# Optimization experiments

Hardware: AMD Instinct MI355X
Metric: run time of the kernel (lower is better)

The kernel has to match this reference:

```python
import jax, jax.numpy as jnp
import numpy as np

D = 1024
HID = D // 2          # 512
HLEN = 15
IN_DIM = 4
B, N = 32, 512
EPS = 1e-5


def setup_inputs() -> dict:
    key = jax.random.key(0)
    ks = jax.random.split(key, 16)
    inp = {
        "tokens": jax.random.normal(ks[0], (B, N, D), dtype=jnp.float32),
        "history_traj": jax.random.normal(ks[1], (B, N, HLEN, IN_DIM), dtype=jnp.float32),
        "history_abs": jax.random.normal(ks[2], (B, N, 2), dtype=jnp.float32),
        "ego_speed": jax.random.uniform(ks[3], (B,), dtype=jnp.float32),
        "gps_confidence": jax.random.uniform(ks[4], (B,), dtype=jnp.float32),
        # LSTM params (PyTorch layout: gates stacked i,f,g,o along dim 0)
        "W_ih": jax.random.normal(ks[5], (4 * HID, IN_DIM), dtype=jnp.float32) * (1.0 / np.sqrt(IN_DIM)),
        "W_hh": jax.random.normal(ks[6], (4 * HID, HID), dtype=jnp.float32) * (1.0 / np.sqrt(HID)),
        "b_ih": jnp.zeros((4 * HID,), dtype=jnp.float32),
        "b_hh": jnp.zeros((4 * HID,), dtype=jnp.float32),
        "W_rel": jax.random.normal(ks[7], (D, HID), dtype=jnp.float32) * (0.1 / np.sqrt(HID)),
        "W_abs": jax.random.normal(ks[8], (D, 2), dtype=jnp.float32) * 0.1,
        "W_g1": jax.random.normal(ks[9], (16, 2), dtype=jnp.float32) * 0.5,
        "b_g1": jnp.zeros((16,), dtype=jnp.float32),
        "W_g2": jax.random.normal(ks[10], (1, 16), dtype=jnp.float32) * 0.25,
        "b_g2": jnp.zeros((1,), dtype=jnp.float32),
        "gamma": jnp.ones((D,), dtype=jnp.float32),
        "beta": jnp.zeros((D,), dtype=jnp.float32),
    }
    return inp


def _lstm_final_hidden(x, W_ih, W_hh, b_ih, b_hh):
    """x: (BN, H, in) -> final hidden state (BN, HID). PyTorch gate order i,f,g,o."""
    BN = x.shape[0]
    # precompute input contribution for all steps: (H, BN, 4*HID)
    xg = jnp.einsum('bhi,gi->hbg', x, W_ih) + (b_ih + b_hh)

    def step(carry, xg_t):
        h, c = carry
        gates = xg_t + h @ W_hh.T  # (BN, 4*HID)
        i, f, g, o = jnp.split(gates, 4, axis=-1)
        i = jax.nn.sigmoid(i)
        f = jax.nn.sigmoid(f)
        g = jnp.tanh(g)
        o = jax.nn.sigmoid(o)
        c = f * c + i * g
        h = o * jnp.tanh(c)
        return (h, c), None

    h0 = jnp.zeros((BN, HID), dtype=x.dtype)
    c0 = jnp.zeros((BN, HID), dtype=x.dtype)
    (h, _), _ = jax.lax.scan(step, (h0, c0), xg)
    return h


def reference(tokens, history_traj, history_abs, ego_speed, gps_confidence,
              W_ih, W_hh, b_ih, b_hh, W_rel, W_abs, W_g1, b_g1, W_g2, b_g2,
              gamma, beta):
    Bv, Nv, Dv = tokens.shape
    Hv = history_traj.shape[2]
    traj_flat = history_traj.reshape(Bv * Nv, Hv, -1)
    h_n = _lstm_final_hidden(traj_flat, W_ih, W_hh, b_ih, b_hh)  # (B*N, HID)
    h_rel = (h_n @ W_rel.T).reshape(Bv, Nv, Dv)                  # (B, N, D)
    h_abs = history_abs @ W_abs.T                                # (B, N, D)
    conf = jnp.stack([ego_speed, gps_confidence], axis=-1)       # (B, 2)
    gate = jax.nn.relu(conf @ W_g1.T + b_g1) @ W_g2.T + b_g2     # (B, 1)
    alpha = jax.nn.sigmoid(gate)[:, None, :]                     # (B, 1, 1)
    h_fused = alpha * h_rel + (1.0 - alpha) * h_abs
    x = tokens + h_fused
    mu = jnp.mean(x, axis=-1, keepdims=True)
    var = jnp.mean(jnp.square(x - mu), axis=-1, keepdims=True)
    return (x - mu) * jax.lax.rsqrt(var + EPS) * gamma + beta
```

## Files before the change

### kernel.cpp

```cpp
#include <hip/hip_runtime.h>
#include <hip/hip_bf16.h>
#include <math.h>

#define BB 32
#define NN 512
#define BN 16384
#define DD 1024
#define HID 512
#define G4 2048
#define HLEN 15
#define IND 4
#define EPS 1e-5f

typedef __bf16 v8bf __attribute__((ext_vector_type(8)));
typedef float  v4f  __attribute__((ext_vector_type(4)));

__device__ __forceinline__ void async_copy16(const __bf16* gsrc, __bf16* ldst) {
    __builtin_amdgcn_global_load_lds(
        (const __attribute__((address_space(1))) void*)gsrc,
        (__attribute__((address_space(3))) void*)ldst, 16, 0, 0);
}

#define VMCNTI(n) asm volatile("s_waitcnt vmcnt(" #n ")" ::: "memory")
#define VMCNT0 VMCNTI(0)
#define LGKM0  asm volatile("s_waitcnt lgkmcnt(0)" ::: "memory")
#define MEMFENCE asm volatile("" ::: "memory")

#define LOG2E 1.44269504f
__device__ __forceinline__ float sigmf(float x) {
    return __builtin_amdgcn_rcpf(1.0f + __builtin_amdgcn_exp2f(-LOG2E * x));
}
__device__ __forceinline__ float tanh_fast(float x) {
    return 1.0f - 2.0f * __builtin_amdgcn_rcpf(1.0f + __builtin_amdgcn_exp2f(2.0f * LOG2E * x));
}

__global__ void convert_w(const float* __restrict__ Whh, const float* __restrict__ Wrel,
                          const float* __restrict__ Wih, const float* __restrict__ bih,
                          const float* __restrict__ bhh,
                          __bf16* __restrict__ whh_b, __bf16* __restrict__ wrel_b,
                          float* __restrict__ wih_i, float* __restrict__ bsum) {
    int i = blockIdx.x * 256 + threadIdx.x;
    if (i < G4 * HID) whh_b[i] = (__bf16)Whh[i];
    if (i < DD * HID) wrel_b[i] = (__bf16)Wrel[i];
    if (i < G4) {
        int uu = i >> 2, gi = i & 3;
        int src = gi * HID + uu;
        wih_i[i * 4 + 0] = Wih[src * 4 + 0];
        wih_i[i * 4 + 1] = Wih[src * 4 + 1];
        wih_i[i * 4 + 2] = Wih[src * 4 + 2];
        wih_i[i * 4 + 3] = Wih[src * 4 + 3];
        bsum[i] = bih[src] + bhh[src];
    }
}

__global__ void alpha_kernel(const float* __restrict__ es, const float* __restrict__ gc,
                             const float* __restrict__ W_g1, const float* __restrict__ b_g1,
                             const float* __restrict__ W_g2, const float* __restrict__ b_g2,
                             float* __restrict__ alpha) {
    int b = threadIdx.x;
    if (b >= BB) return;
    float c0 = es[b], c1 = gc[b];
    float acc = b_g2[0];
    for (int k = 0; k < 16; ++k) {
        float hk = c0 * W_g1[k * 2] + c1 * W_g1[k * 2 + 1] + b_g1[k];
        hk = fmaxf(hk, 0.0f);
        acc += hk * W_g2[k];
    }
    alpha[b] = 1.0f / (1.0f + expf(-acc));
}

__global__ __launch_bounds__(256) void lstm_cell0(const float* __restrict__ traj,
                                                  const float* __restrict__ wih_i,
                                                  const float* __restrict__ bsum,
                                                  float* __restrict__ c,
                                                  __bf16* __restrict__ h) {
    int idx = blockIdx.x * 256 + threadIdx.x;
    int row = idx >> 9;
    float4 x = *(const float4*)(traj + (size_t)row * (HLEN * IND));
    int u = idx & 511;
    float g[4];
    #pragma unroll
    for (int gi = 0; gi < 4; ++gi) {
        int j = u * 4 + gi;
        float4 w = *(const float4*)(wih_i + (size_t)j * 4);
        g[gi] = bsum[j] + w.x * x.x + w.y * x.y + w.z * x.z + w.w * x.w;
    }
    float ig = sigmf(g[0]);
    float gg = tanh_fast(g[2]);
    float og = sigmf(g[3]);
    float cn = ig * gg;
    c[idx] = cn;
    h[idx] = (__bf16)(og * tanh_fast(cn));
}


__device__ __forceinline__ void bar_acq() {
    __builtin_amdgcn_s_barrier();
    LGKM0;
    __builtin_amdgcn_sched_barrier(0);
}
__device__ __forceinline__ void bar_rel() {
    __builtin_amdgcn_s_barrier();
    MEMFENCE;
}

template<int IG, int GH, bool RA, bool RB>
__device__ __forceinline__ void phase_read(const __bf16* smb, int wave_m, int wn,
                                           int mrow, int pcs,
                                           v8bf (&ar)[4][2], v8bf (&br)[2][2][2]) {
    if (RA) {
        #pragma unroll
        for (int ii = 0; ii < 4; ++ii)
            #pragma unroll
            for (int ks = 0; ks < 2; ++ks)
                ar[ii][ks] = *(const v8bf*)(smb +
                    (wave_m * 128 + IG * 64 + ii * 16 + mrow) * 64 + ((ks * 32) ^ pcs));
    }
    if (RB) {
        #pragma unroll
        for (int g2 = 0; g2 < 2; ++g2)
            #pragma unroll
            for (int ks = 0; ks < 2; ++ks)
                br[GH][g2][ks] = *(const v8bf*)(smb + 16384 +
                    ((GH * 2 + g2) * 64 + wn * 16 + mrow) * 64 + ((ks * 32) ^ pcs));
    }
}

template<int IG, int GH>
__device__ __forceinline__ void phase_mfma(v8bf (&ar)[4][2], v8bf (&br)[2][2][2],
                                           v4f (&acc)[8][4]) {
    __builtin_amdgcn_s_setprio(1);
    #pragma unroll
    for (int ii = 0; ii < 4; ++ii)
        #pragma unroll
        for (int g2 = 0; g2 < 2; ++g2)
            #pragma unroll
            for (int ks = 0; ks < 2; ++ks)
                acc[IG * 4 + ii][GH * 2 + g2] = __builtin_amdgcn_mfma_f32_16x16x32_bf16(
                    ar[ii][ks], br[GH][g2][ks], acc[IG * 4 + ii][GH * 2 + g2], 0, 0, 0);
    __builtin_amdgcn_s_setprio(0);
}

#define STAGE_A(buf, kt) do {                                        \
    async_copy16(pa[0] + (kt) * 64, &sm[buf][wb]);                   \
    async_copy16(pa[1] + (kt) * 64, &sm[buf][wb + 4096]);            \
    async_copy16(pa[2] + (kt) * 64, &sm[buf][wb + 8192]);            \
    async_copy16(pa[3] + (kt) * 64, &sm[buf][wb + 12288]); } while (0)
#define STAGE_BLO(buf, kt) do {                                      \
    async_copy16(pb[0] + (kt) * 64, &sm[buf][16384 + wb]);           \
    async_copy16(pb[1] + (kt) * 64, &sm[buf][16384 + wb + 4096]); } while (0)
#define STAGE_BHI(buf, kt) do {                                      \
    async_copy16(pb[2] + (kt) * 64, &sm[buf][16384 + wb + 8192]);    \
    async_copy16(pb[3] + (kt) * 64, &sm[buf][16384 + wb + 12288]); } while (0)

#define GEMM256_BODY                                                               \
    v4f  acc[8][4] = {};                                                           \
    v8bf ar[4][2];                                                                 \
    v8bf br[2][2][2];                                                              \
    STAGE_A(0, 0); STAGE_BLO(0, 0); STAGE_BHI(0, 0);                               \
    VMCNTI(2);                                                                     \
    __builtin_amdgcn_s_barrier();                                                  \
    MEMFENCE;                                                                      \
    _Pragma("unroll")                                                              \
    for (int kt = 0; kt < 7; ++kt) {                                               \
        const int nb = (kt & 1) ^ 1;                                               \
        const __bf16* smb = &sm[kt & 1][0];                                        \
        phase_read<0, 0, true, true>(smb, wave_m, wn, mrow, pcs, ar, br);          \
        if (nb) { STAGE_A(1, kt + 1); } else { STAGE_A(0, kt + 1); }               \
        bar_acq();  phase_mfma<0, 0>(ar, br, acc);  bar_rel();                     \
        phase_read<1, 0, true, false>(smb, wave_m, wn, mrow, pcs, ar, br);         \
        if (nb) { STAGE_BLO(1, kt + 1); } else { STAGE_BLO(0, kt + 1); }           \
        VMCNTI(6);                                                                 \
        bar_acq();  phase_mfma<1, 0>(ar, br, acc);  bar_rel();                     \
        phase_read<1, 1, false, true>(smb, wave_m, wn, mrow, pcs, ar, br);         \
        if (nb) { STAGE_BHI(1, kt + 1); } else { STAGE_BHI(0, kt + 1); }           \
        bar_acq();  phase_mfma<1, 1>(ar, br, acc);  bar_rel();                     \
        phase_read<0, 1, true, false>(smb, wave_m, wn, mrow, pcs, ar, br);         \
        VMCNTI(2);                                                                 \
        bar_acq();  phase_mfma<0, 1>(ar, br, acc);  bar_rel();                     \
    }                                                                              \
    VMCNT0;                                                                        \
    __builtin_amdgcn_s_barrier();                                                  \
    MEMFENCE;                                                                      \
    {                                                                              \
        const __bf16* smb = &sm[1][0];                                             \
        phase_read<0, 0, true, true >(smb, wave_m, wn, mrow, pcs, ar, br);         \
        LGKM0; __builtin_amdgcn_sched_barrier(0);  phase_mfma<0, 0>(ar, br, acc);  \
        phase_read<1, 0, true, false>(smb, wave_m, wn, mrow, pcs, ar, br);         \
        LGKM0; __builtin_amdgcn_sched_barrier(0);  phase_mfma<1, 0>(ar, br, acc);  \
        phase_read<1, 1, false, true>(smb, wave_m, wn, mrow, pcs, ar, br);         \
        LGKM0; __builtin_amdgcn_sched_barrier(0);  phase_mfma<1, 1>(ar, br, acc);  \
        phase_read<0, 1, true, false>(smb, wave_m, wn, mrow, pcs, ar, br);         \
        LGKM0; __builtin_amdgcn_sched_barrier(0);  phase_mfma<0, 1>(ar, br, acc);  \
    }

__global__ __launch_bounds__(512, 2) void gemm_lstm(const __bf16* __restrict__ A,
                                                    const __bf16* __restrict__ Bm,
                                                    const float* __restrict__ traj,
                                                    const float* __restrict__ wih_i,
                                                    const float* __restrict__ bsum,
                                                    float* __restrict__ c,
                                                    __bf16* __restrict__ h_out,
                                                    int t) {
    __shared__ __bf16 sm[2][32768];

    const int tid    = threadIdx.x;
    const int lane   = tid & 63;
    const int wave   = tid >> 6;
    const int wave_m = wave & 1;
    const int wn     = wave >> 1;
    const int bm     = blockIdx.x;
    const int ub     = blockIdx.y;

    const int mrow = lane & 15;
    const int pcs  = (((lane >> 4) ^ (mrow & 7)) << 3);

    const __bf16* pa[4];
    const __bf16* pb[4];
    #pragma unroll
    for (int s = 0; s < 4; ++s) {
        const int ca = tid + s * 512;
        const int r  = ca >> 3;
        const int l  = (ca & 7) ^ (r & 7);
        pa[s] = A + (size_t)(bm * 256 + r) * HID + l * 8;
        const int g = r >> 6, ul = r & 63;
        pb[s] = Bm + (size_t)(g * HID + ub * 64 + ul) * HID + l * 8;
    }
    const int wb = wave * 512;

    GEMM256_BODY

    const int u_glob = ub * 64 + wn * 16 + mrow;
    const int crow4  = (lane >> 4) * 4;
    float wv[4][4], bs4[4];
    #pragma unroll
    for (int gi = 0; gi < 4; ++gi) {
        float4 wp = *(const float4*)(wih_i + (size_t)(u_glob * 4 + gi) * 4);
        wv[gi][0] = wp.x; wv[gi][1] = wp.y; wv[gi][2] = wp.z; wv[gi][3] = wp.w;
        bs4[gi] = bsum[u_glob * 4 + gi];
    }
    #pragma unroll
    for (int i = 0; i < 8; ++i) {
        const int growb = bm * 256 + wave_m * 128 + (i >> 2) * 64 + (i & 3) * 16 + crow4;
        #pragma unroll
        for (int r = 0; r < 4; ++r) {
            const int grow = growb + r;
            const float4 x = *(const float4*)(traj + (size_t)grow * (HLEN * IND) + t * IND);
            float g[4];
            #pragma unroll
            for (int gi = 0; gi < 4; ++gi)
                g[gi] = acc[i][gi][r] + bs4[gi]
                      + wv[gi][0] * x.x + wv[gi][1] * x.y + wv[gi][2] * x.z + wv[gi][3] * x.w;
            float ig = sigmf(g[0]);
            float fg = sigmf(g[1]);
            float gg = tanh_fast(g[2]);
            float og = sigmf(g[3]);
            size_t ci = (size_t)grow * HID + u_glob;
            float cn = fg * c[ci] + ig * gg;
            c[ci] = cn;
            h_out[ci] = (__bf16)(og * tanh_fast(cn));
        }
    }
}

__global__ __launch_bounds__(512, 2) void gemm_proj(const __bf16* __restrict__ A,
                                                    const __bf16* __restrict__ Bm,
                                                    __bf16* __restrict__ Cout) {
    __shared__ __bf16 sm[2][32768];

    const int tid    = threadIdx.x;
    const int lane   = tid & 63;
    const int wave   = tid >> 6;
    const int wave_m = wave & 1;
    const int wn     = wave >> 1;
    const int bm     = blockIdx.x;
    const int bn     = blockIdx.y;

    const int mrow = lane & 15;
    const int pcs  = (((lane >> 4) ^ (mrow & 7)) << 3);

    const __bf16* pa[4];
    const __bf16* pb[4];
    #pragma unroll
    for (int s = 0; s < 4; ++s) {
        const int ca = tid + s * 512;
        const int r  = ca >> 3;
        const int l  = (ca & 7) ^ (r & 7);
        pa[s] = A  + (size_t)(bm * 256 + r) * HID + l * 8;
        pb[s] = Bm + (size_t)(bn * 256 + r) * HID + l * 8;
    }
    const int wb = wave * 512;

    GEMM256_BODY

    const int crow4 = (lane >> 4) * 4;
    #pragma unroll
    for (int i = 0; i < 8; ++i) {
        const int growb = bm * 256 + wave_m * 128 + (i >> 2) * 64 + (i & 3) * 16 + crow4;
        #pragma unroll
        for (int j = 0; j < 4; ++j) {
            const int gcol = bn * 256 + j * 64 + wn * 16 + mrow;
            #pragma unroll
            for (int r = 0; r < 4; ++r)
                Cout[(size_t)(growb + r) * DD + gcol] = (__bf16)acc[i][j][r];
        }
    }
}

__global__ __launch_bounds__(256) void fuse_ln(const float* __restrict__ tokens,
                                               const __bf16* __restrict__ hrel,
                                               const float* __restrict__ habs_in,
                                               const float* __restrict__ W_abs,
                                               const float* __restrict__ alpha,
                                               const float* __restrict__ gamma,
                                               const float* __restrict__ beta,
                                               float* __restrict__ out) {
    const int row = blockIdx.x;
    const int b   = row >> 9;
    const float al = alpha[b];
    const float a0 = habs_in[(size_t)row * 2];
    const float a1 = habs_in[(size_t)row * 2 + 1];
    const int tid  = threadIdx.x;
    const int lane = tid & 63;
    const int wave = tid >> 6;

    __shared__ float red[4];

    float x[4];
    float s = 0.0f;
    #pragma unroll
    for (int q = 0; q < 4; ++q) {
        int dcol = tid + q * 256;
        float habs = a0 * W_abs[dcol * 2] + a1 * W_abs[dcol * 2 + 1];
        float v = tokens[(size_t)row * DD + dcol]
                + al * (float)hrel[(size_t)row * DD + dcol]
                + (1.0f - al) * habs;
        x[q] = v;
        s += v;
    }
    #pragma unroll
    for (int off = 32; off > 0; off >>= 1) s += __shfl_down(s, off);
    if (lane == 0) red[wave] = s;
    __syncthreads();
    float mu = (red[0] + red[1] + red[2] + red[3]) * (1.0f / DD);

    float vs = 0.0f;
    #pragma unroll
    for (int q = 0; q < 4; ++q) {
        float d = x[q] - mu;
        vs += d * d;
    }
    #pragma unroll
    for (int off = 32; off > 0; off >>= 1) vs += __shfl_down(vs, off);
    __syncthreads();
    if (lane == 0) red[wave] = vs;
    __syncthreads();
    float var = (red[0] + red[1] + red[2] + red[3]) * (1.0f / DD);
    float rstd = rsqrtf(var + EPS);

    #pragma unroll
    for (int q = 0; q < 4; ++q) {
        int dcol = tid + q * 256;
        out[(size_t)row * DD + dcol] = (x[q] - mu) * rstd * gamma[dcol] + beta[dcol];
    }
}

extern "C" void kernel_launch(void* const* d_in, const int* in_sizes, int n_in,
                              void* d_out, int out_size, void* d_ws, size_t ws_size,
                              hipStream_t stream) {
    const float* tokens   = (const float*)d_in[0];
    const float* traj     = (const float*)d_in[1];
    const float* habs     = (const float*)d_in[2];
    const float* espeed   = (const float*)d_in[3];
    const float* gconf    = (const float*)d_in[4];
    const float* W_ih     = (const float*)d_in[5];
    const float* W_hh     = (const float*)d_in[6];
    const float* b_ih     = (const float*)d_in[7];
    const float* b_hh     = (const float*)d_in[8];
    const float* W_rel    = (const float*)d_in[9];
    const float* W_abs    = (const float*)d_in[10];
    const float* W_g1     = (const float*)d_in[11];
    const float* b_g1     = (const float*)d_in[12];
    const float* W_g2     = (const float*)d_in[13];
    const float* b_g2     = (const float*)d_in[14];
    const float* gamma    = (const float*)d_in[15];
    const float* beta     = (const float*)d_in[16];
    float* out = (float*)d_out;

    char* ws = (char*)d_ws;
    size_t off = 0;
    __bf16* whh_b  = (__bf16*)(ws + off); off += (size_t)G4 * HID * 2;
    __bf16* wrel_b = (__bf16*)(ws + off); off += (size_t)DD * HID * 2;
    float*  wih_i  = (float*)(ws + off);  off += (size_t)G4 * 4 * 4;
    float*  bsum   = (float*)(ws + off);  off += (size_t)G4 * 4;
    __bf16* h0     = (__bf16*)(ws + off); off += (size_t)BN * HID * 2;
    __bf16* h1     = (__bf16*)(ws + off); off += (size_t)BN * HID * 2;
    float*  c      = (float*)(ws + off);  off += (size_t)BN * HID * 4;
    __bf16* hrel   = (__bf16*)(ws + off); off += (size_t)BN * DD * 2;
    float*  alpha  = (float*)(ws + off);  off += 256;

    convert_w<<<(G4 * HID + 255) / 256, 256, 0, stream>>>(W_hh, W_rel, W_ih, b_ih, b_hh,
                                                          whh_b, wrel_b, wih_i, bsum);
    alpha_kernel<<<1, 64, 0, stream>>>(espeed, gconf, W_g1, b_g1, W_g2, b_g2, alpha);
    lstm_cell0<<<(BN * HID) / 256, 256, 0, stream>>>(traj, wih_i, bsum, c, h0);

    __bf16* hbuf[2] = {h0, h1};
    for (int t = 1; t < HLEN; ++t) {
        const __bf16* hin = hbuf[(t + 1) & 1];
        __bf16* hout = hbuf[t & 1];
        gemm_lstm<<<dim3(BN / 256, HID / 64), 512, 0, stream>>>(hin, whh_b, traj, wih_i, bsum,
                                                                c, hout, t);
    }
    gemm_proj<<<dim3(BN / 256, DD / 256), 512, 0, stream>>>(h0, wrel_b, hrel);
    fuse_ln<<<BN, 256, 0, stream>>>(tokens, hrel, habs, W_abs, alpha, gamma, beta, out);
}
```

Before: 868.3 us.

## Shrink GEMM tiles to 128x256 with K=32 double-buffered simple pipeline

Result: slower. 891.3 us (+2.6%).

```diff
diff --git a/kernel.cpp b/kernel.cpp
--- a/kernel.cpp
+++ b/kernel.cpp
@@ -94,107 +94,7 @@
 }
 
 
-__device__ __forceinline__ void bar_acq() {
-    __builtin_amdgcn_s_barrier();
-    LGKM0;
-    __builtin_amdgcn_sched_barrier(0);
-}
-__device__ __forceinline__ void bar_rel() {
-    __builtin_amdgcn_s_barrier();
-    MEMFENCE;
-}
-
-template<int IG, int GH, bool RA, bool RB>
-__device__ __forceinline__ void phase_read(const __bf16* smb, int wave_m, int wn,
-                                           int mrow, int pcs,
-                                           v8bf (&ar)[4][2], v8bf (&br)[2][2][2]) {
-    if (RA) {
-        #pragma unroll
-        for (int ii = 0; ii < 4; ++ii)
-            #pragma unroll
-            for (int ks = 0; ks < 2; ++ks)
-                ar[ii][ks] = *(const v8bf*)(smb +
-                    (wave_m * 128 + IG * 64 + ii * 16 + mrow) * 64 + ((ks * 32) ^ pcs));
-    }
-    if (RB) {
-        #pragma unroll
-        for (int g2 = 0; g2 < 2; ++g2)
-            #pragma unroll
-            for (int ks = 0; ks < 2; ++ks)
-                br[GH][g2][ks] = *(const v8bf*)(smb + 16384 +
-                    ((GH * 2 + g2) * 64 + wn * 16 + mrow) * 64 + ((ks * 32) ^ pcs));
-    }
-}
-
-template<int IG, int GH>
-__device__ __forceinline__ void phase_mfma(v8bf (&ar)[4][2], v8bf (&br)[2][2][2],
-                                           v4f (&acc)[8][4]) {
-    __builtin_amdgcn_s_setprio(1);
-    #pragma unroll
-    for (int ii = 0; ii < 4; ++ii)
-        #pragma unroll
-        for (int g2 = 0; g2 < 2; ++g2)
-            #pragma unroll
-            for (int ks = 0; ks < 2; ++ks)
-                acc[IG * 4 + ii][GH * 2 + g2] = __builtin_amdgcn_mfma_f32_16x16x32_bf16(
-                    ar[ii][ks], br[GH][g2][ks], acc[IG * 4 + ii][GH * 2 + g2], 0, 0, 0);
-    __builtin_amdgcn_s_setprio(0);
-}
-
-#define STAGE_A(buf, kt) do {                                        \
-    async_copy16(pa[0] + (kt) * 64, &sm[buf][wb]);                   \
-    async_copy16(pa[1] + (kt) * 64, &sm[buf][wb + 4096]);            \
-    async_copy16(pa[2] + (kt) * 64, &sm[buf][wb + 8192]);            \
-    async_copy16(pa[3] + (kt) * 64, &sm[buf][wb + 12288]); } while (0)
-#define STAGE_BLO(buf, kt) do {                                      \
-    async_copy16(pb[0] + (kt) * 64, &sm[buf][16384 + wb]);           \
-    async_copy16(pb[1] + (kt) * 64, &sm[buf][16384 + wb + 4096]); } while (0)
-#define STAGE_BHI(buf, kt) do {                                      \
-    async_copy16(pb[2] + (kt) * 64, &sm[buf][16384 + wb + 8192]);    \
-    async_copy16(pb[3] + (kt) * 64, &sm[buf][16384 + wb + 12288]); } while (0)
-
-#define GEMM256_BODY                                                               \
-    v4f  acc[8][4] = {};                                                           \
-    v8bf ar[4][2];                                                                 \
-    v8bf br[2][2][2];                                                              \
-    STAGE_A(0, 0); STAGE_BLO(0, 0); STAGE_BHI(0, 0);                               \
-    VMCNTI(2);                                                                     \
-    __builtin_amdgcn_s_barrier();                                                  \
-    MEMFENCE;                                                                      \
-    _Pragma("unroll")                                                              \
-    for (int kt = 0; kt < 7; ++kt) {                                               \
-        const int nb = (kt & 1) ^ 1;                                               \
-        const __bf16* smb = &sm[kt & 1][0];                                        \
-        phase_read<0, 0, true, true>(smb, wave_m, wn, mrow, pcs, ar, br);          \
-        if (nb) { STAGE_A(1, kt + 1); } else { STAGE_A(0, kt + 1); }               \
-        bar_acq();  phase_mfma<0, 0>(ar, br, acc);  bar_rel();                     \
-        phase_read<1, 0, true, false>(smb, wave_m, wn, mrow, pcs, ar, br);         \
-        if (nb) { STAGE_BLO(1, kt + 1); } else { STAGE_BLO(0, kt + 1); }           \
-        VMCNTI(6);                                                                 \
-        bar_acq();  phase_mfma<1, 0>(ar, br, acc);  bar_rel();                     \
-        phase_read<1, 1, false, true>(smb, wave_m, wn, mrow, pcs, ar, br);         \
-        if (nb) { STAGE_BHI(1, kt + 1); } else { STAGE_BHI(0, kt + 1); }           \
-        bar_acq();  phase_mfma<1, 1>(ar, br, acc);  bar_rel();                     \
-        phase_read<0, 1, true, false>(smb, wave_m, wn, mrow, pcs, ar, br);         \
-        VMCNTI(2);                                                                 \
-        bar_acq();  phase_mfma<0, 1>(ar, br, acc);  bar_rel();                     \
-    }                                                                              \
-    VMCNT0;                                                                        \
-    __builtin_amdgcn_s_barrier();                                                  \
-    MEMFENCE;                                                                      \
-    {                                                                              \
-        const __bf16* smb = &sm[1][0];                                             \
-        phase_read<0, 0, true, true >(smb, wave_m, wn, mrow, pcs, ar, br);         \
-        LGKM0; __builtin_amdgcn_sched_barrier(0);  phase_mfma<0, 0>(ar, br, acc);  \
-        phase_read<1, 0, true, false>(smb, wave_m, wn, mrow, pcs, ar, br);         \
-        LGKM0; __builtin_amdgcn_sched_barrier(0);  phase_mfma<1, 0>(ar, br, acc);  \
-        phase_read<1, 1, false, true>(smb, wave_m, wn, mrow, pcs, ar, br);         \
-        LGKM0; __builtin_amdgcn_sched_barrier(0);  phase_mfma<1, 1>(ar, br, acc);  \
-        phase_read<0, 1, true, false>(smb, wave_m, wn, mrow, pcs, ar, br);         \
-        LGKM0; __builtin_amdgcn_sched_barrier(0);  phase_mfma<0, 1>(ar, br, acc);  \
-    }
-
-__global__ __launch_bounds__(512, 2) void gemm_lstm(const __bf16* __restrict__ A,
+__global__ __launch_bounds__(512, 4) void gemm_lstm(const __bf16* __restrict__ A,
                                                     const __bf16* __restrict__ Bm,
                                                     const float* __restrict__ traj,
                                                     const float* __restrict__ wih_i,
@@ -202,7 +102,7 @@
                                                     float* __restrict__ c,
                                                     __bf16* __restrict__ h_out,
                                                     int t) {
-    __shared__ __bf16 sm[2][32768];
+    __shared__ __bf16 sm[2][12288];
 
     const int tid    = threadIdx.x;
     const int lane   = tid & 63;
@@ -211,26 +111,61 @@
     const int wn     = wave >> 1;
     const int bm     = blockIdx.x;
     const int ub     = blockIdx.y;
+    const int u0     = ub * 64;
 
     const int mrow = lane & 15;
-    const int pcs  = (((lane >> 4) ^ (mrow & 7)) << 3);
-
-    const __bf16* pa[4];
-    const __bf16* pb[4];
-    #pragma unroll
-    for (int s = 0; s < 4; ++s) {
+    const int pcs  = (((lane >> 4) ^ ((mrow >> 1) & 3)) << 3);
+
+    const int rA = tid >> 2;
+    const int lA_ = (tid & 3) ^ ((rA >> 1) & 3);
+    const __bf16* pa = A + (size_t)(bm * 128 + rA) * HID + lA_ * 8;
+    const __bf16* pb[2];
+    #pragma unroll
+    for (int s = 0; s < 2; ++s) {
         const int ca = tid + s * 512;
-        const int r  = ca >> 3;
-        const int l  = (ca & 7) ^ (r & 7);
-        pa[s] = A + (size_t)(bm * 256 + r) * HID + l * 8;
-        const int g = r >> 6, ul = r & 63;
-        pb[s] = Bm + (size_t)(g * HID + ub * 64 + ul) * HID + l * 8;
+        const int r  = ca >> 2;
+        const int l  = (ca & 3) ^ ((r >> 1) & 3);
+        pb[s] = Bm + (size_t)((r >> 6) * HID + u0 + (r & 63)) * HID + l * 8;
     }
     const int wb = wave * 512;
 
-    GEMM256_BODY
-
-    const int u_glob = ub * 64 + wn * 16 + mrow;
+    #define STAGE(buf, kt) do {                                      \
+        async_copy16(pa    + (kt) * 32, &sm[buf][wb]);               \
+        async_copy16(pb[0] + (kt) * 32, &sm[buf][4096 + wb]);        \
+        async_copy16(pb[1] + (kt) * 32, &sm[buf][8192 + wb]); } while (0)
+
+    v4f acc[4][4] = {};
+
+    STAGE(0, 0);
+    #pragma unroll
+    for (int kt = 0; kt < 16; ++kt) {
+        const int cb = kt & 1;
+        if (kt < 15) { STAGE(cb ^ 1, kt + 1); VMCNTI(3); } else { VMCNT0; }
+        __builtin_amdgcn_s_barrier();
+        MEMFENCE;
+        const __bf16* smb = &sm[cb][0];
+        v8bf ar[4], br[4];
+        #pragma unroll
+        for (int ii = 0; ii < 4; ++ii)
+            ar[ii] = *(const v8bf*)(smb + (wave_m * 64 + ii * 16 + mrow) * 32 + pcs);
+        #pragma unroll
+        for (int j = 0; j < 4; ++j)
+            br[j] = *(const v8bf*)(smb + 4096 + (j * 64 + wn * 16 + mrow) * 32 + pcs);
+        LGKM0;
+        __builtin_amdgcn_sched_barrier(0);
+        __builtin_amdgcn_s_setprio(1);
+        #pragma unroll
+        for (int ii = 0; ii < 4; ++ii)
+            #pragma unroll
+            for (int j = 0; j < 4; ++j)
+                acc[ii][j] = __builtin_amdgcn_mfma_f32_16x16x32_bf16(ar[ii], br[j], acc[ii][j], 0, 0, 0);
+        __builtin_amdgcn_s_setprio(0);
+        __builtin_amdgcn_s_barrier();
+        MEMFENCE;
+    }
+    #undef STAGE
+
+    const int u_glob = u0 + wn * 16 + mrow;
     const int crow4  = (lane >> 4) * 4;
     float wv[4][4], bs4[4];
     #pragma unroll
@@ -240,8 +175,8 @@
         bs4[gi] = bsum[u_glob * 4 + gi];
     }
     #pragma unroll
-    for (int i = 0; i < 8; ++i) {
-        const int growb = bm * 256 + wave_m * 128 + (i >> 2) * 64 + (i & 3) * 16 + crow4;
+    for (int ii = 0; ii < 4; ++ii) {
+        const int growb = bm * 128 + wave_m * 64 + ii * 16 + crow4;
         #pragma unroll
         for (int r = 0; r < 4; ++r) {
             const int grow = growb + r;
@@ -249,7 +184,7 @@
             float g[4];
             #pragma unroll
             for (int gi = 0; gi < 4; ++gi)
-                g[gi] = acc[i][gi][r] + bs4[gi]
+                g[gi] = acc[ii][gi][r] + bs4[gi]
                       + wv[gi][0] * x.x + wv[gi][1] * x.y + wv[gi][2] * x.z + wv[gi][3] * x.w;
             float ig = sigmf(g[0]);
             float fg = sigmf(g[1]);
@@ -263,10 +198,10 @@
     }
 }
 
-__global__ __launch_bounds__(512, 2) void gemm_proj(const __bf16* __restrict__ A,
+__global__ __launch_bounds__(512, 4) void gemm_proj(const __bf16* __restrict__ A,
                                                     const __bf16* __restrict__ Bm,
                                                     __bf16* __restrict__ Cout) {
-    __shared__ __bf16 sm[2][32768];
+    __shared__ __bf16 sm[2][12288];
 
     const int tid    = threadIdx.x;
     const int lane   = tid & 63;
@@ -277,32 +212,67 @@
     const int bn     = blockIdx.y;
 
     const int mrow = lane & 15;
-    const int pcs  = (((lane >> 4) ^ (mrow & 7)) << 3);
-
-    const __bf16* pa[4];
-    const __bf16* pb[4];
-    #pragma unroll
-    for (int s = 0; s < 4; ++s) {
+    const int pcs  = (((lane >> 4) ^ ((mrow >> 1) & 3)) << 3);
+
+    const int rA = tid >> 2;
+    const int lA_ = (tid & 3) ^ ((rA >> 1) & 3);
+    const __bf16* pa = A + (size_t)(bm * 128 + rA) * HID + lA_ * 8;
+    const __bf16* pb[2];
+    #pragma unroll
+    for (int s = 0; s < 2; ++s) {
         const int ca = tid + s * 512;
-        const int r  = ca >> 3;
-        const int l  = (ca & 7) ^ (r & 7);
-        pa[s] = A  + (size_t)(bm * 256 + r) * HID + l * 8;
+        const int r  = ca >> 2;
+        const int l  = (ca & 3) ^ ((r >> 1) & 3);
         pb[s] = Bm + (size_t)(bn * 256 + r) * HID + l * 8;
     }
     const int wb = wave * 512;
 
-    GEMM256_BODY
+    #define STAGE(buf, kt) do {                                      \
+        async_copy16(pa    + (kt) * 32, &sm[buf][wb]);               \
+        async_copy16(pb[0] + (kt) * 32, &sm[buf][4096 + wb]);        \
+        async_copy16(pb[1] + (kt) * 32, &sm[buf][8192 + wb]); } while (0)
+
+    v4f acc[4][4] = {};
+
+    STAGE(0, 0);
+    #pragma unroll
+    for (int kt = 0; kt < 16; ++kt) {
+        const int cb = kt & 1;
+        if (kt < 15) { STAGE(cb ^ 1, kt + 1); VMCNTI(3); } else { VMCNT0; }
+        __builtin_amdgcn_s_barrier();
+        MEMFENCE;
+        const __bf16* smb = &sm[cb][0];
+        v8bf ar[4], br[4];
+        #pragma unroll
+        for (int ii = 0; ii < 4; ++ii)
+            ar[ii] = *(const v8bf*)(smb + (wave_m * 64 + ii * 16 + mrow) * 32 + pcs);
+        #pragma unroll
+        for (int j = 0; j < 4; ++j)
+            br[j] = *(const v8bf*)(smb + 4096 + (j * 64 + wn * 16 + mrow) * 32 + pcs);
+        LGKM0;
+        __builtin_amdgcn_sched_barrier(0);
+        __builtin_amdgcn_s_setprio(1);
+        #pragma unroll
+        for (int ii = 0; ii < 4; ++ii)
+            #pragma unroll
+            for (int j = 0; j < 4; ++j)
+                acc[ii][j] = __builtin_amdgcn_mfma_f32_16x16x32_bf16(ar[ii], br[j], acc[ii][j], 0, 0, 0);
+        __builtin_amdgcn_s_setprio(0);
+        __builtin_amdgcn_s_barrier();
+        MEMFENCE;
+    }
+    #undef STAGE
 
     const int crow4 = (lane >> 4) * 4;
     #pragma unroll
-    for (int i = 0; i < 8; ++i) {
-        const int growb = bm * 256 + wave_m * 128 + (i >> 2) * 64 + (i & 3) * 16 + crow4;
+    for (int ii = 0; ii < 4; ++ii) {
+        const int growb = bm * 128 + wave_m * 64 + ii * 16 + crow4;
         #pragma unroll
         for (int j = 0; j < 4; ++j) {
             const int gcol = bn * 256 + j * 64 + wn * 16 + mrow;
             #pragma unroll
             for (int r = 0; r < 4; ++r)
-                Cout[(size_t)(growb + r) * DD + gcol] = (__bf16)acc[i][j][r];
+                Cout[(size_t)(growb + r) * DD + gcol] = (__bf16)acc[ii][j][r];
         }
     }
 }
@@ -408,9 +378,9 @@
     for (int t = 1; t < HLEN; ++t) {
         const __bf16* hin = hbuf[(t + 1) & 1];
         __bf16* hout = hbuf[t & 1];
-        gemm_lstm<<<dim3(BN / 256, HID / 64), 512, 0, stream>>>(hin, whh_b, traj, wih_i, bsum,
+        gemm_lstm<<<dim3(BN / 128, HID / 64), 512, 0, stream>>>(hin, whh_b, traj, wih_i, bsum,
                                                                 c, hout, t);
     }
-    gemm_proj<<<dim3(BN / 256, DD / 256), 512, 0, stream>>>(h0, wrel_b, hrel);
+    gemm_proj<<<dim3(BN / 128, DD / 256), 512, 0, stream>>>(h0, wrel_b, hrel);
     fuse_ln<<<BN, 256, 0, stream>>>(tokens, hrel, habs, W_abs, alpha, gamma, beta, out);
 }
```
